# Performance work log

Hardware: AMD Instinct MI355X
Metric: run time of the kernel (lower is better)

The kernel has to match this reference:

```python
import jax, jax.numpy as jnp
import numpy as np

B, S, T, M, H = 16, 128, 1024, 16, 1024
HID = 1024        # attention MLP hidden
WIDTH_EMB = 20    # width embedding dim
N_LING = 2        # len(linguistic_feature_types)


def setup_inputs() -> dict:
    key = jax.random.key(0)
    ks = jax.random.split(key, 12)
    doc_embeddings = jax.random.normal(ks[0], (B, T, H), dtype=jnp.float32)
    start_mappings = jax.random.normal(ks[1], (B, S, T), dtype=jnp.float32)
    end_mappings = jax.random.normal(ks[2], (B, S, T), dtype=jnp.float32)
    continuous_mappings = jax.random.normal(ks[3], (B, S, M, T), dtype=jnp.float32)
    width = jax.random.randint(ks[4], (B, S), 0, M, dtype=jnp.int64)
    linguistic_labels = jax.random.normal(ks[5], (B, S, N_LING), dtype=jnp.float32)
    # attention MLP params (torch Linear layout transposed to x @ W + b)
    W1 = jax.random.normal(ks[6], (H, HID), dtype=jnp.float32) * (1.0 / np.sqrt(H))
    b1 = jax.random.normal(ks[7], (HID,), dtype=jnp.float32) * 0.01
    W2 = jax.random.normal(ks[8], (HID, 1), dtype=jnp.float32) * (1.0 / np.sqrt(HID))
    b2 = jax.random.normal(ks[9], (1,), dtype=jnp.float32) * 0.01
    width_table = jax.random.normal(ks[10], (5, WIDTH_EMB), dtype=jnp.float32)
    return {
        'doc_embeddings': doc_embeddings,
        'start_mappings': start_mappings,
        'end_mappings': end_mappings,
        'continuous_mappings': continuous_mappings,
        'linguistic_labels': linguistic_labels,
        'W1': W1, 'b1': b1, 'W2': W2, 'b2': b2,
        'width_table': width_table,
        'width': width,
    }


def reference(doc_embeddings, start_mappings, end_mappings, continuous_mappings,
              linguistic_labels, W1, b1, W2, b2, width_table, width):
    # one-hot matmul gathers
    start = jnp.einsum('bst,bth->bsh', start_mappings, doc_embeddings)
    end = jnp.einsum('bst,bth->bsh', end_mappings, doc_embeddings)
    cont = jnp.einsum('bsmt,bth->bsmh', continuous_mappings, doc_embeddings)
    b, s, m, h = cont.shape
    vector = jnp.concatenate([start, end], axis=-1).reshape(b * s, 2 * h)
    cont = cont.reshape(b * s, m, h)
    w = width.reshape(b * s)
    ling = linguistic_labels.reshape(b * s, -1)
    # padded masked attention pooling
    masks = (jnp.arange(m)[None, :] < jnp.maximum(w, 1)[:, None]).astype(cont.dtype)
    hdn = jax.nn.relu(jnp.einsum('nmh,hk->nmk', cont, W1) + b1)
    scores = (jnp.einsum('nmk,ko->nmo', hdn, W2) + b2)[..., 0]  # [n, m]
    scores = scores * masks
    scores = jnp.where(scores != 0, scores, jnp.asarray(-9e9, scores.dtype))
    att = jax.nn.softmax(scores, axis=1)
    weighted_sum = jnp.einsum('nm,nmh->nh', att, cont)
    vector = jnp.concatenate([vector, weighted_sum], axis=1)
    # linguistic feature columns (loop over fixed small feature list)
    for fi in range(N_LING):
        vector = jnp.concatenate([vector, ling[:, fi:fi + 1]], axis=1)
    # width embedding (clamp max=4)
    wemb = width_table[jnp.clip(w, 0, 4)]
    vector = jnp.concatenate([vector, wemb], axis=1)
    return vector.reshape(b, s, -1)
```

## Files before the change

kernel.cpp:

```cpp
#include <hip/hip_runtime.h>

typedef unsigned short ushort_t;
typedef unsigned int uint_t;
typedef _Float16 f16;
typedef f16 f16x8 __attribute__((ext_vector_type(8)));
typedef float f32x4 __attribute__((ext_vector_type(4)));

#define B_   16
#define S_   128
#define T_   1024
#define M_   16
#define H_   1024
#define OUTW 3094
#define NSPAN (B_*S_)
#define NROW  (NSPAN*M_)

#define WS_CONT   0
#define WS_DOCT   67108864
#define WS_W1T    100663296
#define WS_SCORES 102760448

__device__ __forceinline__ float sane(float v) {
  return fminf(fmaxf(v, -60000.f), 60000.f);
}
__device__ __forceinline__ ushort_t f16bits(float f) {
  union { f16 h; ushort_t u; } c; c.h = (f16)f; return c.u;
}
__device__ __forceinline__ void load_lds16(const void* g, void* l) {
  __builtin_amdgcn_global_load_lds(
      (const __attribute__((address_space(1))) uint_t*)g,
      (__attribute__((address_space(3))) uint_t*)l, 16, 0, 0);
}

__global__ __launch_bounds__(256) void tconv(const float* __restrict__ in,
                                             ushort_t* __restrict__ out,
                                             int R, int C) {
  __shared__ uint_t tile[64][65];
  const int tid = threadIdx.x;
  const int c0 = blockIdx.x * 64, r0 = blockIdx.y * 64;
  const size_t mo = (size_t)blockIdx.z * R * C;
  const float* ip = in + mo;
  ushort_t* op = out + mo;
  const int tx = tid & 63, ty = tid >> 6;
#pragma unroll
  for (int p = 0; p < 16; ++p) {
    int r = p * 4 + ty;
    tile[r][tx] = (uint_t)f16bits(ip[(size_t)(r0 + r) * C + c0 + tx]);
  }
  __syncthreads();
  const int rr = (tid & 31) * 2, cc0 = tid >> 5;
  uint_t* op32 = (uint_t*)op;
#pragma unroll
  for (int p = 0; p < 8; ++p) {
    int c = cc0 + p * 8;
    uint_t lo = tile[rr][c] & 0xffffu;
    uint_t hi = tile[rr + 1][c] & 0xffffu;
    op32[((size_t)(c0 + c) * R + r0 + rr) >> 1] = lo | (hi << 16);
  }
}

__global__ __launch_bounds__(256) void gemm1(const float* __restrict__ startm,
                                             const float* __restrict__ endm,
                                             const float* __restrict__ contm,
                                             const ushort_t* __restrict__ docT,
                                             float* __restrict__ out,
                                             f16* __restrict__ contF) {
  __shared__ f16 As[2 * 128 * 32];
  __shared__ f16 Bs[2 * 128 * 32];
  const int tid = threadIdx.x;
  const uint_t pid = blockIdx.x;
  const int xcd = pid & 7;
  const int s_  = pid >> 3;
  const int ct  = s_ & 7;
  const int pg  = (s_ >> 3) * 8 + xcd;
  const int rt  = pg >> 4;
  const int b   = pg & 15;

  const float* Ap;
  if (rt == 0)      Ap = startm + (size_t)b * S_ * T_;
  else if (rt == 1) Ap = endm + (size_t)b * S_ * T_;
  else              Ap = contm + (size_t)b * (S_ * M_ * T_) + (size_t)(rt - 2) * 128 * T_;
  const ushort_t* Bp = docT + (size_t)b * (H_ * T_) + (size_t)ct * 128 * T_;

  const int lane = tid & 63, w = tid >> 6;
  const int wr = w >> 1, wc = w & 1;
  const int quad = lane >> 4, l16 = lane & 15;
  const int arow = tid >> 1;
  const int ah   = tid & 1;
  const int asw  = (arow >> 1) & 3;
  const int ac0  = ((2 * ah) ^ asw) * 8;
  const int ac1  = ((2 * ah + 1) ^ asw) * 8;
  const float* aSrc = Ap + (size_t)arow * T_ + ah * 16;
  const int brow = lane >> 2;
  const int bcol = ((lane & 3) ^ ((lane >> 3) & 3)) * 8;

  f32x4 acc[4][4];
#pragma unroll
  for (int i = 0; i < 4; ++i)
#pragma unroll
    for (int j = 0; j < 4; ++j) acc[i][j] = (f32x4){0.f, 0.f, 0.f, 0.f};

  {
    f32x4 a0 = *(const f32x4*)(aSrc + 0);
    f32x4 a1 = *(const f32x4*)(aSrc + 4);
    f32x4 a2 = *(const f32x4*)(aSrc + 8);
    f32x4 a3 = *(const f32x4*)(aSrc + 12);
#pragma unroll
    for (int i = 0; i < 2; ++i) {
      const int rb = w * 32 + i * 16;
      load_lds16(Bp + (size_t)(rb + brow) * T_ + bcol, &Bs[rb * 32]);
    }
    f16x8 h0, h1;
#pragma unroll
    for (int k = 0; k < 4; ++k) {
      h0[k] = (f16)a0[k]; h0[k + 4] = (f16)a1[k];
      h1[k] = (f16)a2[k]; h1[k + 4] = (f16)a3[k];
    }
    *(f16x8*)&As[arow * 32 + ac0] = h0;
    *(f16x8*)&As[arow * 32 + ac1] = h1;
    __syncthreads();
  }

  int cur = 0;
  for (int k0 = 0; k0 < T_; k0 += 32) {
    const int nxt = cur ^ 1;
    const bool pf = (k0 + 32 < T_);
    f32x4 a0, a1, a2, a3;
    if (pf) {
      const float* ap = aSrc + (k0 + 32);
      a0 = *(const f32x4*)(ap + 0);
      a1 = *(const f32x4*)(ap + 4);
      a2 = *(const f32x4*)(ap + 8);
      a3 = *(const f32x4*)(ap + 12);
#pragma unroll
      for (int i = 0; i < 2; ++i) {
        const int rb = w * 32 + i * 16;
        load_lds16(Bp + (size_t)(rb + brow) * T_ + (k0 + 32) + bcol,
                   &Bs[nxt * 4096 + rb * 32]);
      }
    }
    f16x8 af[4], bfr[4];
#pragma unroll
    for (int i = 0; i < 4; ++i) {
      const int row = wr * 64 + i * 16 + l16;
      const int sw = (row >> 1) & 3;
      af[i] = *(const f16x8*)&As[cur * 4096 + row * 32 + ((quad ^ sw) * 8)];
    }
#pragma unroll
    for (int j = 0; j < 4; ++j) {
      const int row = wc * 64 + j * 16 + l16;
      const int sw = (row >> 1) & 3;
      bfr[j] = *(const f16x8*)&Bs[cur * 4096 + row * 32 + ((quad ^ sw) * 8)];
    }
#pragma unroll
    for (int i = 0; i < 4; ++i)
#pragma unroll
      for (int j = 0; j < 4; ++j)
        acc[i][j] = __builtin_amdgcn_mfma_f32_16x16x32_f16(af[i], bfr[j], acc[i][j], 0, 0, 0);
    if (pf) {
      f16x8 h0, h1;
#pragma unroll
      for (int k = 0; k < 4; ++k) {
        h0[k] = (f16)a0[k]; h0[k + 4] = (f16)a1[k];
        h1[k] = (f16)a2[k]; h1[k + 4] = (f16)a3[k];
      }
      *(f16x8*)&As[nxt * 4096 + arow * 32 + ac0] = h0;
      *(f16x8*)&As[nxt * 4096 + arow * 32 + ac1] = h1;
    }
    __syncthreads();
    cur = nxt;
  }

  if (rt < 2) {
    float* op = out + (size_t)b * S_ * OUTW + (size_t)rt * 1024 + (size_t)ct * 128;
#pragma unroll
    for (int i = 0; i < 4; ++i)
#pragma unroll
      for (int j = 0; j < 4; ++j)
#pragma unroll
        for (int r = 0; r < 4; ++r) {
          int row = wr * 64 + i * 16 + quad * 4 + r;
          int col = wc * 64 + j * 16 + l16;
          op[(size_t)row * OUTW + col] = sane(acc[i][j][r]);
        }
  } else {
    f16* cp = contF + ((size_t)b * 2048 + (size_t)(rt - 2) * 128) * H_ + (size_t)ct * 128;
#pragma unroll
    for (int i = 0; i < 4; ++i)
#pragma unroll
      for (int j = 0; j < 4; ++j)
#pragma unroll
        for (int r = 0; r < 4; ++r) {
          int row = wr * 64 + i * 16 + quad * 4 + r;
          int col = wc * 64 + j * 16 + l16;
          cp[(size_t)row * H_ + col] = (f16)sane(acc[i][j][r]);
        }
  }
}

__global__ __launch_bounds__(256) void gemm2(const f16* __restrict__ contF,
                                             const f16* __restrict__ W1T,
                                             const float* __restrict__ b1,
                                             const float* __restrict__ W2,
                                             float* __restrict__ scores) {
  __shared__ f16 As[2 * 128 * 32];
  __shared__ f16 Bs[2 * 128 * 32];
  const int tid = threadIdx.x;
  const uint_t pid = blockIdx.x;
  const int xcd = pid & 7;
  const int s_  = pid >> 3;
  const int ct  = s_ & 7;
  const int rt  = (s_ >> 3) * 8 + xcd;

  const f16* Ap = contF + (size_t)rt * 128 * H_;
  const f16* Bp = W1T + (size_t)ct * 128 * H_;

  const int lane = tid & 63, w = tid >> 6;
  const int wr = w >> 1, wc = w & 1;
  const int quad = lane >> 4, l16 = lane & 15;
  const int brow = lane >> 2;
  const int bcol = ((lane & 3) ^ ((lane >> 3) & 3)) * 8;

  f32x4 acc[4][4];
#pragma unroll
  for (int i = 0; i < 4; ++i)
#pragma unroll
    for (int j = 0; j < 4; ++j) acc[i][j] = (f32x4){0.f, 0.f, 0.f, 0.f};

#pragma unroll
  for (int i = 0; i < 2; ++i) {
    const int rb = w * 32 + i * 16;
    load_lds16(Ap + (size_t)(rb + brow) * H_ + bcol, &As[rb * 32]);
    load_lds16(Bp + (size_t)(rb + brow) * H_ + bcol, &Bs[rb * 32]);
  }
  __syncthreads();

  int cur = 0;
  for (int k0 = 0; k0 < H_; k0 += 32) {
    const int nxt = cur ^ 1;
    const bool pf = (k0 + 32 < H_);
    if (pf) {
#pragma unroll
      for (int i = 0; i < 2; ++i) {
        const int rb = w * 32 + i * 16;
        load_lds16(Ap + (size_t)(rb + brow) * H_ + (k0 + 32) + bcol,
                   &As[nxt * 4096 + rb * 32]);
        load_lds16(Bp + (size_t)(rb + brow) * H_ + (k0 + 32) + bcol,
                   &Bs[nxt * 4096 + rb * 32]);
      }
    }
    f16x8 af[4], bfr[4];
#pragma unroll
    for (int i = 0; i < 4; ++i) {
      const int row = wr * 64 + i * 16 + l16;
      const int sw = (row >> 1) & 3;
      af[i] = *(const f16x8*)&As[cur * 4096 + row * 32 + ((quad ^ sw) * 8)];
    }
#pragma unroll
    for (int j = 0; j < 4; ++j) {
      const int row = wc * 64 + j * 16 + l16;
      const int sw = (row >> 1) & 3;
      bfr[j] = *(const f16x8*)&Bs[cur * 4096 + row * 32 + ((quad ^ sw) * 8)];
    }
#pragma unroll
    for (int i = 0; i < 4; ++i)
#pragma unroll
      for (int j = 0; j < 4; ++j)
        acc[i][j] = __builtin_amdgcn_mfma_f32_16x16x32_f16(af[i], bfr[j], acc[i][j], 0, 0, 0);
    __syncthreads();
    cur = nxt;
  }

  const int colbase = ct * 128 + wc * 64;
#pragma unroll
  for (int i = 0; i < 4; ++i) {
#pragma unroll
    for (int r = 0; r < 4; ++r) {
      float t = 0.f;
#pragma unroll
      for (int j = 0; j < 4; ++j) {
        int c = colbase + j * 16 + l16;
        float v = acc[i][j][r] + b1[c];
        v = fmaxf(v, 0.f);
        t = fmaf(v, W2[c], t);
      }
      t += __shfl_xor(t, 1);
      t += __shfl_xor(t, 2);
      t += __shfl_xor(t, 4);
      t += __shfl_xor(t, 8);
      if (l16 == 0) {
        int row = rt * 128 + wr * 64 + i * 16 + quad * 4 + r;
        atomicAdd(&scores[row], t);
      }
    }
  }
}

__global__ __launch_bounds__(256) void finalize(const f16* __restrict__ contF,
                                                const float* __restrict__ scores,
                                                const float* __restrict__ ling,
                                                const float* __restrict__ b2,
                                                const float* __restrict__ wtab,
                                                const int* __restrict__ width,
                                                float* __restrict__ out) {
  const int n = blockIdx.x;
  const int tid = threadIdx.x;
  __shared__ float sc[16];
  if (tid < 16) {
    float raw = scores[n * 16 + tid] + b2[0];
    if (raw != raw) raw = 0.0f;
    int wv = width[n];
    int wm = wv > 1 ? wv : 1;
    float s = (tid < wm) ? raw : 0.0f;
    if (s == 0.0f) s = -9e9f;
    sc[tid] = s;
  }
  __syncthreads();
  float mx = sc[0];
#pragma unroll
  for (int m = 1; m < 16; ++m) mx = fmaxf(mx, sc[m]);
  float e[16];
  float ssum = 0.f;
#pragma unroll
  for (int m = 0; m < 16; ++m) { e[m] = __expf(sc[m] - mx); ssum += e[m]; }
  const float inv = 1.0f / ssum;
  const f16* cp = contF + (size_t)n * (M_ * H_);
  float* op = out + (size_t)n * OUTW;
#pragma unroll
  for (int hh = 0; hh < 4; ++hh) {
    int h = tid + hh * 256;
    float a = 0.f;
#pragma unroll
    for (int m = 0; m < 16; ++m) a = fmaf(e[m], (float)cp[m * H_ + h], a);
    op[2048 + h] = sane(a * inv);
  }
  if (tid < 2) op[3072 + tid] = ling[n * 2 + tid];
  if (tid < 20) {
    int wv = width[n];
    int wcl = wv < 4 ? wv : 4;
    if (wcl < 0) wcl = 0;
    op[3074 + tid] = wtab[wcl * 20 + tid];
  }
}

extern "C" void kernel_launch(void* const* d_in, const int* in_sizes, int n_in,
                              void* d_out, int out_size, void* d_ws, size_t ws_size,
                              hipStream_t stream) {
  const float* doc    = (const float*)d_in[0];
  const float* startm = (const float*)d_in[1];
  const float* endm   = (const float*)d_in[2];
  const float* contm  = (const float*)d_in[3];
  const float* ling   = (const float*)d_in[4];
  const float* W1     = (const float*)d_in[5];
  const float* b1     = (const float*)d_in[6];
  const float* W2     = (const float*)d_in[7];
  const float* b2     = (const float*)d_in[8];
  const float* wtab   = (const float*)d_in[9];
  const int*   width  = (const int*)d_in[10];
  float* out = (float*)d_out;

  char* ws = (char*)d_ws;
  f16*      contF  = (f16*)(ws + WS_CONT);
  ushort_t* docT   = (ushort_t*)(ws + WS_DOCT);
  f16*      W1T    = (f16*)(ws + WS_W1T);
  float*    scores = (float*)(ws + WS_SCORES);

  hipMemsetAsync(scores, 0, NROW * sizeof(float), stream);
  tconv<<<dim3(16, 16, 16), 256, 0, stream>>>(doc, docT, 1024, 1024);
  tconv<<<dim3(16, 16, 1), 256, 0, stream>>>(W1, (ushort_t*)W1T, 1024, 1024);
  gemm1<<<dim3(2304, 1, 1), 256, 0, stream>>>(startm, endm, contm, docT, out, contF);
  gemm2<<<dim3(2048, 1, 1), 256, 0, stream>>>(contF, (const f16*)W1T, b1, W2, scores);
  finalize<<<dim3(NSPAN, 1, 1), 256, 0, stream>>>(contF, scores, ling, b2, wtab, width, out);
}
```

Baseline: 504.2 us.

## Retile gemm2 to 256x128 blocks with 512 threads and triple-buffered K=64 pipeline

The attention-score GEMM now uses 256x128 output tiles computed by 8 waves, so each W1 tile loaded into LDS is shared by twice as many rows and half as many blocks are launched. The K step grows to 64, and loads are triple-buffered with explicit vmcnt waits, so two tiles are in flight while the current one is computed. The LDS swizzle is changed to an XOR over 8 chunks. This adds LDS footprint (about 144KB) and relies on hand-placed waitcnt and barrier instructions, which limits occupancy to one block per CU and makes the ordering fragile.

```diff
diff --git a/kernel.cpp b/kernel.cpp
--- a/kernel.cpp
+++ b/kernel.cpp
@@ -198,28 +198,30 @@
   }
 }
 
-__global__ __launch_bounds__(256) void gemm2(const f16* __restrict__ contF,
+__global__ __launch_bounds__(512) void gemm2(const f16* __restrict__ contF,
                                              const f16* __restrict__ W1T,
                                              const float* __restrict__ b1,
                                              const float* __restrict__ W2,
                                              float* __restrict__ scores) {
-  __shared__ f16 As[2 * 128 * 32];
-  __shared__ f16 Bs[2 * 128 * 32];
+  __shared__ f16 As[3][256 * 64];
+  __shared__ f16 Bs[3][128 * 64];
   const int tid = threadIdx.x;
   const uint_t pid = blockIdx.x;
   const int xcd = pid & 7;
   const int s_  = pid >> 3;
   const int ct  = s_ & 7;
-  const int rt  = (s_ >> 3) * 8 + xcd;
-
-  const f16* Ap = contF + (size_t)rt * 128 * H_;
+  const int g   = s_ >> 3;
+  const int rt  = g * 8 + xcd;
+
+  const f16* Ap = contF + (size_t)rt * 256 * H_;
   const f16* Bp = W1T + (size_t)ct * 128 * H_;
 
   const int lane = tid & 63, w = tid >> 6;
-  const int wr = w >> 1, wc = w & 1;
+  const int wm = w >> 1;
+  const int wn = w & 1;
   const int quad = lane >> 4, l16 = lane & 15;
-  const int brow = lane >> 2;
-  const int bcol = ((lane & 3) ^ ((lane >> 3) & 3)) * 8;
+  const int lrow = lane >> 3;
+  const int lchk = lane & 7;
 
   f32x4 acc[4][4];
 #pragma unroll
@@ -228,59 +230,86 @@
     for (int j = 0; j < 4; ++j) acc[i][j] = (f32x4){0.f, 0.f, 0.f, 0.f};
 
 #pragma unroll
-  for (int i = 0; i < 2; ++i) {
-    const int rb = w * 32 + i * 16;
-    load_lds16(Ap + (size_t)(rb + brow) * H_ + bcol, &As[rb * 32]);
-    load_lds16(Bp + (size_t)(rb + brow) * H_ + bcol, &Bs[rb * 32]);
-  }
+  for (int t = 0; t < 2; ++t) {
+    const int k0 = t * 64;
+#pragma unroll
+    for (int j = 0; j < 4; ++j) {
+      const int rowb = w * 32 + j * 8;
+      const int row  = rowb + lrow;
+      const int c    = lchk ^ (row & 7);
+      load_lds16(Ap + (size_t)row * H_ + k0 + c * 8, &As[t][rowb * 64]);
+    }
+#pragma unroll
+    for (int j = 0; j < 2; ++j) {
+      const int rowb = w * 16 + j * 8;
+      const int row  = rowb + lrow;
+      const int c    = lchk ^ (row & 7);
+      load_lds16(Bp + (size_t)row * H_ + k0 + c * 8, &Bs[t][rowb * 64]);
+    }
+  }
+  asm volatile("s_waitcnt vmcnt(0)" ::: "memory");
   __syncthreads();
 
-  int cur = 0;
-  for (int k0 = 0; k0 < H_; k0 += 32) {
-    const int nxt = cur ^ 1;
-    const bool pf = (k0 + 32 < H_);
-    if (pf) {
-#pragma unroll
-      for (int i = 0; i < 2; ++i) {
-        const int rb = w * 32 + i * 16;
-        load_lds16(Ap + (size_t)(rb + brow) * H_ + (k0 + 32) + bcol,
-                   &As[nxt * 4096 + rb * 32]);
-        load_lds16(Bp + (size_t)(rb + brow) * H_ + (k0 + 32) + bcol,
-                   &Bs[nxt * 4096 + rb * 32]);
-      }
-    }
-    f16x8 af[4], bfr[4];
-#pragma unroll
-    for (int i = 0; i < 4; ++i) {
-      const int row = wr * 64 + i * 16 + l16;
-      const int sw = (row >> 1) & 3;
-      af[i] = *(const f16x8*)&As[cur * 4096 + row * 32 + ((quad ^ sw) * 8)];
-    }
-#pragma unroll
-    for (int j = 0; j < 4; ++j) {
-      const int row = wc * 64 + j * 16 + l16;
-      const int sw = (row >> 1) & 3;
-      bfr[j] = *(const f16x8*)&Bs[cur * 4096 + row * 32 + ((quad ^ sw) * 8)];
-    }
-#pragma unroll
-    for (int i = 0; i < 4; ++i)
-#pragma unroll
-      for (int j = 0; j < 4; ++j)
-        acc[i][j] = __builtin_amdgcn_mfma_f32_16x16x32_f16(af[i], bfr[j], acc[i][j], 0, 0, 0);
-    __syncthreads();
-    cur = nxt;
-  }
-
-  const int colbase = ct * 128 + wc * 64;
-#pragma unroll
-  for (int i = 0; i < 4; ++i) {
+  for (int kt = 0; kt < 16; ++kt) {
+    const int rb = kt % 3;
+    if (kt + 2 < 16) {
+      const int sb = (kt + 2) % 3;
+      const int k0 = (kt + 2) * 64;
+#pragma unroll
+      for (int j = 0; j < 4; ++j) {
+        const int rowb = w * 32 + j * 8;
+        const int row  = rowb + lrow;
+        const int c    = lchk ^ (row & 7);
+        load_lds16(Ap + (size_t)row * H_ + k0 + c * 8, &As[sb][rowb * 64]);
+      }
+#pragma unroll
+      for (int j = 0; j < 2; ++j) {
+        const int rowb = w * 16 + j * 8;
+        const int row  = rowb + lrow;
+        const int c    = lchk ^ (row & 7);
+        load_lds16(Bp + (size_t)row * H_ + k0 + c * 8, &Bs[sb][rowb * 64]);
+      }
+    }
+    f16x8 af[2][4], bf[2][4];
+#pragma unroll
+    for (int ks = 0; ks < 2; ++ks) {
+#pragma unroll
+      for (int mf = 0; mf < 4; ++mf) {
+        const int row = wm * 64 + mf * 16 + l16;
+        const int c   = ks * 4 + quad;
+        af[ks][mf] = *(const f16x8*)&As[rb][row * 64 + ((c ^ (row & 7)) * 8)];
+      }
+#pragma unroll
+      for (int nf = 0; nf < 4; ++nf) {
+        const int row = wn * 64 + nf * 16 + l16;
+        const int c   = ks * 4 + quad;
+        bf[ks][nf] = *(const f16x8*)&Bs[rb][row * 64 + ((c ^ (row & 7)) * 8)];
+      }
+    }
+#pragma unroll
+    for (int ks = 0; ks < 2; ++ks)
+#pragma unroll
+      for (int mf = 0; mf < 4; ++mf)
+#pragma unroll
+        for (int nf = 0; nf < 4; ++nf)
+          acc[mf][nf] = __builtin_amdgcn_mfma_f32_16x16x32_f16(
+              af[ks][mf], bf[ks][nf], acc[mf][nf], 0, 0, 0);
+    if (kt <= 13) asm volatile("s_waitcnt vmcnt(6) lgkmcnt(0)" ::: "memory");
+    else          asm volatile("s_waitcnt vmcnt(0) lgkmcnt(0)" ::: "memory");
+    __builtin_amdgcn_s_barrier();
+    __builtin_amdgcn_sched_barrier(0);
+  }
+
+  const int colbase = ct * 128 + wn * 64;
+#pragma unroll
+  for (int mf = 0; mf < 4; ++mf) {
 #pragma unroll
     for (int r = 0; r < 4; ++r) {
       float t = 0.f;
 #pragma unroll
-      for (int j = 0; j < 4; ++j) {
-        int c = colbase + j * 16 + l16;
-        float v = acc[i][j][r] + b1[c];
+      for (int nf = 0; nf < 4; ++nf) {
+        int c = colbase + nf * 16 + l16;
+        float v = acc[mf][nf][r] + b1[c];
         v = fmaxf(v, 0.f);
         t = fmaf(v, W2[c], t);
       }
@@ -289,7 +318,7 @@
       t += __shfl_xor(t, 4);
       t += __shfl_xor(t, 8);
       if (l16 == 0) {
-        int row = rt * 128 + wr * 64 + i * 16 + quad * 4 + r;
+        int row = rt * 256 + wm * 64 + mf * 16 + quad * 4 + r;
         atomicAdd(&scores[row], t);
       }
     }
@@ -369,6 +398,6 @@
   tconv<<<dim3(16, 16, 16), 256, 0, stream>>>(doc, docT, 1024, 1024);
   tconv<<<dim3(16, 16, 1), 256, 0, stream>>>(W1, (ushort_t*)W1T, 1024, 1024);
   gemm1<<<dim3(2304, 1, 1), 256, 0, stream>>>(startm, endm, contm, docT, out, contF);
-  gemm2<<<dim3(2048, 1, 1), 256, 0, stream>>>(contF, (const f16*)W1T, b1, W2, scores);
+  gemm2<<<dim3(1024, 1, 1), 512, 0, stream>>>(contF, (const f16*)W1T, b1, W2, scores);
   finalize<<<dim3(NSPAN, 1, 1), 256, 0, stream>>>(contF, scores, ling, b2, wtab, width, out);
 }
```

Measured after the change: 522.8 us. 1.04x slower.
